# Optimization experiments

Measured on AMD Instinct MI355X. Metric: run time of the kernel, lower is better.

Reference implementation:

```python
import jax, jax.numpy as jnp
import numpy as np

MAX_FREQ = 4
OMEGA = 0.5 * np.pi
PATCH = 64


def _unnorm(c, size):
    # align_corners=False convention of torch.grid_sample
    return ((c + 1.0) * size - 1.0) / 2.0


def _gather(im, yy, xx):
    # im [C,H,W], yy/xx [Ho,Wo] -> [C,Ho,Wo]
    return im[:, yy, xx]


def _gs_nearest(inp, grid):
    # inp [B,C,H,W], grid [B,Ho,Wo,2] (x,y); padding_mode='border'
    B, C, H, W = inp.shape
    x = jnp.clip(jnp.round(_unnorm(grid[..., 0], W)), 0, W - 1).astype(jnp.int32)
    y = jnp.clip(jnp.round(_unnorm(grid[..., 1], H)), 0, H - 1).astype(jnp.int32)
    return jax.vmap(_gather)(inp, y, x)  # [B,C,Ho,Wo]


def _gs_bilinear(inp, grid):
    B, C, H, W = inp.shape
    x = jnp.clip(_unnorm(grid[..., 0], W), 0.0, W - 1.0)
    y = jnp.clip(_unnorm(grid[..., 1], H), 0.0, H - 1.0)
    x0 = jnp.floor(x); y0 = jnp.floor(y)
    wx = (x - x0)[:, None]; wy = (y - y0)[:, None]  # [B,1,Ho,Wo]
    x0i = x0.astype(jnp.int32); y0i = y0.astype(jnp.int32)
    x1i = jnp.minimum(x0i + 1, W - 1); y1i = jnp.minimum(y0i + 1, H - 1)
    g = jax.vmap(_gather)
    v00 = g(inp, y0i, x0i); v01 = g(inp, y0i, x1i)
    v10 = g(inp, y1i, x0i); v11 = g(inp, y1i, x1i)
    return (v00 * (1 - wx) * (1 - wy) + v01 * wx * (1 - wy)
            + v10 * (1 - wx) * wy + v11 * wx * wy)


def _conv2d(x, w, b):
    y = jax.lax.conv_general_dilated(x, w, (1, 1), ((1, 1), (1, 1)),
                                     dimension_numbers=("NCHW", "OIHW", "NCHW"))
    return y + b[None, :, None, None]


def _lc_decoder(q, rel):
    # q [B,Ho,Wo,2F+1], rel [B,Ho,Wo,1]; Fourier basis [1, cos(k*w*rel), sin(k*w*rel)]
    k = jnp.arange(1, MAX_FREQ + 1, dtype=q.dtype)
    ang = rel * k * OMEGA  # [B,Ho,Wo,F]
    basis = jnp.concatenate([jnp.ones_like(rel), jnp.cos(ang), jnp.sin(ang)], axis=-1)
    return jnp.sum(q * basis, axis=-1, keepdims=True)  # [B,Ho,Wo,1]


def _forward(sinogram, feat, grid, square_inv, adapt_w, adapt_b):
    B = feat.shape[0]
    sino = _conv2d(feat, adapt_w, adapt_b)          # [B,2F+1,V,D]
    V, D = sino.shape[-2], sino.shape[-1]
    # make_coord along detector axis (dim=1 coord channel), padding=0
    coord_d = ((jnp.arange(D, dtype=sino.dtype) + 0.5) / D) * 2.0 - 1.0
    sino_coord = jnp.broadcast_to(coord_d[None, None, None, :], (B, 1, V, D))
    shift_interval = 1.0 / D
    eps = 1e-4
    q_recons, lengths = [], []
    for sx in (-shift_interval, shift_interval):  # ensembling shifts
        g = grid + jnp.array([sx, 0.0], dtype=grid.dtype) + 1e-6
        q_recon = jnp.transpose(_gs_nearest(sino, g), (0, 2, 3, 1))       # [B,V,P2,2F+1]
        q_coord = jnp.transpose(_gs_nearest(sino_coord, g), (0, 2, 3, 1))  # [B,V,P2,1]
        rel = (grid[..., 0:1] - q_coord) * D
        q_recons.append(_lc_decoder(q_recon, rel))
        lengths.append(jnp.abs(rel) + eps)
    tot = lengths[0] + lengths[1]
    # lengths are swapped before weighting (cross weighting)
    recon = q_recons[0] * lengths[1] / tot + q_recons[1] * lengths[0] / tot
    out = jnp.sum(jnp.transpose(recon, (0, 3, 1, 2)) * square_inv * 10000.0, axis=-2)
    # back projection of center channel of raw sinogram
    ch = sinogram.shape[1]
    bp = _gs_bilinear(sinogram[:, ch // 2:ch // 2 + 1], grid)
    out = out + jnp.sum(bp * square_inv * 10000.0, axis=-2)  # [B,1,P2]
    return out.reshape(B, 1, PATCH, PATCH)


def setup_inputs() -> dict:
    key = jax.random.key(0)
    ks = jax.random.split(key, 6)
    B, V, D, ENC = 4, 360, 512, 64
    P2 = PATCH * PATCH
    CH = 2 * MAX_FREQ + 1
    return {
        "sinogram": jax.random.normal(ks[0], (B, 1, V, D), jnp.float32),
        "feat": jax.random.normal(ks[1], (B, ENC, V, D), jnp.float32),
        "grid": jax.random.uniform(ks[2], (B, V, P2, 2), jnp.float32, -1.0, 1.0),
        "square_inv": jax.random.uniform(ks[3], (B, 1, V, P2), jnp.float32, 1e-5, 1e-4),
        "adapt_w": jax.random.normal(ks[4], (CH, ENC, 3, 3), jnp.float32) * 0.05,
        "adapt_b": jax.random.normal(ks[5], (CH,), jnp.float32) * 0.05,
    }


def reference(sinogram, feat, grid, square_inv, adapt_w, adapt_b):
    return _forward(sinogram, feat, grid, square_inv, adapt_w, adapt_b)
```

## Files before the change

### kernel.cpp

```cpp
#include <hip/hip_runtime.h>
#include <hip/hip_fp16.h>
#include <math.h>

#define B   4
#define V   360
#define D   512
#define ENC 64
#define CH  9
#define P2  4096
#define NCHUNK 45
#define VCHUNK 8
#define DPT 8
#define RECH 16

__global__ __launch_bounds__(256) void conv_kernel(
    const float* __restrict__ feat,
    const float* __restrict__ w,
    const float* __restrict__ bias,
    __half* __restrict__ sino)
{
    const int bid = blockIdx.x;
    const int sw  = (bid & 7) * 45 + (bid >> 3);
    const int b   = sw / 90;
    const int vt  = sw % 90;
    const int tr  = threadIdx.x >> 6;
    const int v   = vt * 4 + tr;
    const int d0  = (threadIdx.x & 63) * DPT;

    float acc[CH][DPT];
    #pragma unroll
    for (int oc = 0; oc < CH; ++oc) {
        const float bv = bias[oc];
        #pragma unroll
        for (int p = 0; p < DPT; ++p) acc[oc][p] = bv;
    }

    const float* fb = feat + ((size_t)b * ENC * V + v) * D + d0;
    const bool vm = v > 0, vp = v < V - 1;
    const bool dm = d0 > 0, dp = (d0 + DPT) < D;

    for (int ic = 0; ic < ENC; ++ic) {
        const float* f = fb + (size_t)ic * (V * D);
        float r[3][DPT + 2];
        #pragma unroll
        for (int rr = 0; rr < 3; ++rr) {
            const float* fr = f + (rr - 1) * D;
            const bool ok = (rr == 0) ? vm : ((rr == 2) ? vp : true);
            float4 c0 = ok ? *(const float4*)fr       : float4{0.f, 0.f, 0.f, 0.f};
            float4 c1 = ok ? *(const float4*)(fr + 4) : float4{0.f, 0.f, 0.f, 0.f};
            r[rr][1] = c0.x; r[rr][2] = c0.y; r[rr][3] = c0.z; r[rr][4] = c0.w;
            r[rr][5] = c1.x; r[rr][6] = c1.y; r[rr][7] = c1.z; r[rr][8] = c1.w;
            r[rr][0]       = (ok && dm) ? fr[-1]   : 0.f;
            r[rr][DPT + 1] = (ok && dp) ? fr[DPT]  : 0.f;
        }
        #pragma unroll
        for (int oc = 0; oc < CH; ++oc) {
            const float* ww = w + ((size_t)oc * ENC + ic) * 9;
            #pragma unroll
            for (int kr = 0; kr < 3; ++kr) {
                #pragma unroll
                for (int kc = 0; kc < 3; ++kc) {
                    const float wv = ww[kr * 3 + kc];
                    #pragma unroll
                    for (int p = 0; p < DPT; ++p)
                        acc[oc][p] = fmaf(r[kr][p + kc], wv, acc[oc][p]);
                }
            }
        }
    }

    #pragma unroll
    for (int p = 0; p < DPT; ++p) {
        __half* rec = sino + (size_t)(((size_t)b * V + v) * D + d0 + p) * RECH;
        union { __half2 h; unsigned u; } cv;
        uint4 pk;
        cv.h = __floats2half2_rn(acc[0][p], acc[1][p]); pk.x = cv.u;
        cv.h = __floats2half2_rn(acc[2][p], acc[3][p]); pk.y = cv.u;
        cv.h = __floats2half2_rn(acc[4][p], acc[5][p]); pk.z = cv.u;
        cv.h = __floats2half2_rn(acc[6][p], acc[7][p]); pk.w = cv.u;
        *(uint4*)rec = pk;
        cv.h = __floats2half2_rn(acc[8][p], 0.f);
        *(unsigned*)(rec + 8) = cv.u;
    }
}

__device__ __forceinline__ void unpack9(const __half* rec, float* q)
{
    const uint4 a = *(const uint4*)rec;
    union { unsigned u; __half2 h; } c;
    float2 f;
    c.u = a.x; f = __half22float2(c.h); q[0] = f.x; q[1] = f.y;
    c.u = a.y; f = __half22float2(c.h); q[2] = f.x; q[3] = f.y;
    c.u = a.z; f = __half22float2(c.h); q[4] = f.x; q[5] = f.y;
    c.u = a.w; f = __half22float2(c.h); q[6] = f.x; q[7] = f.y;
    const unsigned e = *(const unsigned*)(rec + 8);
    union { unsigned short us; __half hh; } c2;
    c2.us = (unsigned short)e;
    q[8] = __half2float(c2.hh);
}

__device__ __forceinline__ float point_contrib(
    int b, int v, int p,
    const __half* __restrict__ sb, const float* __restrict__ sg,
    const float* __restrict__ grid, const float* __restrict__ sq)
{
    const size_t gi = (size_t)(b * V + v) * P2 + p;
    const double gd = __builtin_nontemporal_load((const double*)grid + gi);
    const unsigned long long gu = __double_as_longlong(gd);
    const float gx = __uint_as_float((unsigned)gu);
    const float gy = __uint_as_float((unsigned)(gu >> 32));
    const float s  = __builtin_nontemporal_load(sq + gi);

    const float fy = ((gy + 1e-6f + 1.f) * (float)V - 1.f) * 0.5f;
    const int   yi = (int)fminf(fmaxf(rintf(fy), 0.f), (float)(V - 1));
    const float fx0 = ((gx + 1e-6f + 1.f) * (float)D - 1.f) * 0.5f;

    float val[2], len[2];
    #pragma unroll
    for (int sft = 0; sft < 2; ++sft) {
        const float fx = (sft == 0) ? (fx0 - 0.5f) : (fx0 + 0.5f);
        const int   xi = (int)fminf(fmaxf(rintf(fx), 0.f), (float)(D - 1));
        const float qc = ((float)xi + 0.5f) * (2.f / (float)D) - 1.f;
        const float rel = (gx - qc) * (float)D;

        float q[9];
        unpack9(sb + (size_t)(yi * D + xi) * RECH, q);

        const float ang = rel * 1.5707963267948966f;
        float s1, c1;
        __sincosf(ang, &s1, &c1);
        const float c2 = fmaf(2.f * c1, c1, -1.f);
        const float s2 = 2.f * c1 * s1;
        const float c3 = fmaf(2.f * c1, c2, -c1);
        const float s3 = fmaf(2.f * c1, s2, -s1);
        const float c4 = fmaf(2.f * c1, c3, -c2);
        const float s4 = fmaf(2.f * c1, s3, -s2);

        float vv = q[0];
        vv = fmaf(q[1], c1, vv); vv = fmaf(q[2], c2, vv);
        vv = fmaf(q[3], c3, vv); vv = fmaf(q[4], c4, vv);
        vv = fmaf(q[5], s1, vv); vv = fmaf(q[6], s2, vv);
        vv = fmaf(q[7], s3, vv); vv = fmaf(q[8], s4, vv);
        val[sft] = vv;
        len[sft] = fabsf(rel) + 1e-4f;
    }
    const float tot   = len[0] + len[1];
    const float recon = (val[0] * len[1] + val[1] * len[0]) / tot;

    float fxb = fminf(fmaxf(((gx + 1.f) * (float)D - 1.f) * 0.5f, 0.f), (float)(D - 1));
    float fyb = fminf(fmaxf(((gy + 1.f) * (float)V - 1.f) * 0.5f, 0.f), (float)(V - 1));
    const float x0 = floorf(fxb), y0 = floorf(fyb);
    const float wx = fxb - x0,    wy = fyb - y0;
    const int x0i = (int)x0, y0i = (int)y0;
    const int x1i = min(x0i + 1, D - 1), y1i = min(y0i + 1, V - 1);
    const float v00 = sg[y0i * D + x0i], v01 = sg[y0i * D + x1i];
    const float v10 = sg[y1i * D + x0i], v11 = sg[y1i * D + x1i];
    const float bp = v00 * (1.f - wx) * (1.f - wy) + v01 * wx * (1.f - wy)
                   + v10 * (1.f - wx) * wy        + v11 * wx * wy;

    return (recon + bp) * s * 1e4f;
}

__global__ __launch_bounds__(256) void sample_kernel(
    const __half* __restrict__ sino,
    const float* __restrict__ sinogram,
    const float* __restrict__ grid,
    const float* __restrict__ sq,
    float* __restrict__ partial)
{
    const int bid = blockIdx.x;
    const int xcd = bid & 7;
    const int b   = xcd >> 1;
    const int idx = ((bid >> 3) << 1) | (xcd & 1);
    const int chunk = idx >> 4;
    const int p  = (idx & 15) * 256 + threadIdx.x;
    const int v0 = chunk * VCHUNK;

    const float* sg = sinogram + (size_t)b * V * D;
    const __half* sb = sino + (size_t)b * V * D * RECH;

    float acc = 0.f;
    #pragma unroll 1
    for (int v = v0; v < v0 + VCHUNK; v += 2) {
        const float c0 = point_contrib(b, v,     p, sb, sg, grid, sq);
        const float c1 = point_contrib(b, v + 1, p, sb, sg, grid, sq);
        acc += c0;
        acc += c1;
    }
    __builtin_nontemporal_store(acc, partial + ((size_t)chunk * B + b) * P2 + p);
}

__global__ __launch_bounds__(256) void reduce_kernel(
    const float* __restrict__ partial, float* __restrict__ out)
{
    const int i = blockIdx.x * 256 + threadIdx.x;
    float a = 0.f;
    #pragma unroll
    for (int c = 0; c < NCHUNK; ++c)
        a += __builtin_nontemporal_load(partial + (size_t)c * B * P2 + i);
    out[i] = a;
}

extern "C" void kernel_launch(void* const* d_in, const int* in_sizes, int n_in,
                              void* d_out, int out_size, void* d_ws, size_t ws_size,
                              hipStream_t stream)
{
    const float* sinogram = (const float*)d_in[0];
    const float* feat     = (const float*)d_in[1];
    const float* grid     = (const float*)d_in[2];
    const float* sq       = (const float*)d_in[3];
    const float* w        = (const float*)d_in[4];
    const float* bias     = (const float*)d_in[5];
    float* out = (float*)d_out;

    __half* sino    = (__half*)d_ws;
    float*  partial = (float*)((char*)d_ws + (size_t)B * V * D * RECH * sizeof(__half));

    conv_kernel<<<dim3(360), 256, 0, stream>>>(feat, w, bias, sino);
    sample_kernel<<<dim3(2880), 256, 0, stream>>>(sino, sinogram, grid, sq, partial);
    reduce_kernel<<<dim3((B * P2) / 256), 256, 0, stream>>>(partial, out);
}
```

Measured before the change: 297.4 us.

## Halve conv tile, batch sample loads, add paired bilinear sinogram table

The conv kernel now computes 4 detector positions per thread over 720 blocks instead of 8 over 360, giving more parallelism and fewer registers per thread. The sample kernel now handles 4 views per block and issues all grid, record and bilinear loads up front before any math, to expose memory-level parallelism. When the workspace is large enough, a precomputed float2 table pairs each sinogram texel with its right neighbour, so bilinear sampling needs two 8-byte loads instead of four scalar ones. This adds an extra kernel launch and doubles the number of partial sums the reduce kernel must read.

```diff
diff --git a/kernel.cpp b/kernel.cpp
--- a/kernel.cpp
+++ b/kernel.cpp
@@ -8,9 +8,9 @@
 #define ENC 64
 #define CH  9
 #define P2  4096
-#define NCHUNK 45
-#define VCHUNK 8
-#define DPT 8
+#define NCHUNK 90
+#define VCHUNK 4
+#define DPT 4
 #define RECH 16
 
 __global__ __launch_bounds__(256) void conv_kernel(
@@ -20,12 +20,12 @@
     __half* __restrict__ sino)
 {
     const int bid = blockIdx.x;
-    const int sw  = (bid & 7) * 45 + (bid >> 3);
-    const int b   = sw / 90;
-    const int vt  = sw % 90;
-    const int tr  = threadIdx.x >> 6;
-    const int v   = vt * 4 + tr;
-    const int d0  = (threadIdx.x & 63) * DPT;
+    const int sw  = (bid & 7) * 90 + (bid >> 3);
+    const int b   = sw / 180;
+    const int vt  = sw % 180;
+    const int tr  = threadIdx.x >> 7;
+    const int v   = vt * 2 + tr;
+    const int d0  = (threadIdx.x & 127) * DPT;
 
     float acc[CH][DPT];
     #pragma unroll
@@ -46,12 +46,10 @@
         for (int rr = 0; rr < 3; ++rr) {
             const float* fr = f + (rr - 1) * D;
             const bool ok = (rr == 0) ? vm : ((rr == 2) ? vp : true);
-            float4 c0 = ok ? *(const float4*)fr       : float4{0.f, 0.f, 0.f, 0.f};
-            float4 c1 = ok ? *(const float4*)(fr + 4) : float4{0.f, 0.f, 0.f, 0.f};
-            r[rr][1] = c0.x; r[rr][2] = c0.y; r[rr][3] = c0.z; r[rr][4] = c0.w;
-            r[rr][5] = c1.x; r[rr][6] = c1.y; r[rr][7] = c1.z; r[rr][8] = c1.w;
-            r[rr][0]       = (ok && dm) ? fr[-1]   : 0.f;
-            r[rr][DPT + 1] = (ok && dp) ? fr[DPT]  : 0.f;
+            float4 c = ok ? *(const float4*)fr : float4{0.f, 0.f, 0.f, 0.f};
+            r[rr][1] = c.x; r[rr][2] = c.y; r[rr][3] = c.z; r[rr][4] = c.w;
+            r[rr][0] = (ok && dm) ? fr[-1]  : 0.f;
+            r[rr][5] = (ok && dp) ? fr[DPT] : 0.f;
         }
         #pragma unroll
         for (int oc = 0; oc < CH; ++oc) {
@@ -84,86 +82,21 @@
     }
 }
 
-__device__ __forceinline__ void unpack9(const __half* rec, float* q)
-{
-    const uint4 a = *(const uint4*)rec;
-    union { unsigned u; __half2 h; } c;
-    float2 f;
-    c.u = a.x; f = __half22float2(c.h); q[0] = f.x; q[1] = f.y;
-    c.u = a.y; f = __half22float2(c.h); q[2] = f.x; q[3] = f.y;
-    c.u = a.z; f = __half22float2(c.h); q[4] = f.x; q[5] = f.y;
-    c.u = a.w; f = __half22float2(c.h); q[6] = f.x; q[7] = f.y;
-    const unsigned e = *(const unsigned*)(rec + 8);
-    union { unsigned short us; __half hh; } c2;
-    c2.us = (unsigned short)e;
-    q[8] = __half2float(c2.hh);
-}
-
-__device__ __forceinline__ float point_contrib(
-    int b, int v, int p,
-    const __half* __restrict__ sb, const float* __restrict__ sg,
-    const float* __restrict__ grid, const float* __restrict__ sq)
-{
-    const size_t gi = (size_t)(b * V + v) * P2 + p;
-    const double gd = __builtin_nontemporal_load((const double*)grid + gi);
-    const unsigned long long gu = __double_as_longlong(gd);
-    const float gx = __uint_as_float((unsigned)gu);
-    const float gy = __uint_as_float((unsigned)(gu >> 32));
-    const float s  = __builtin_nontemporal_load(sq + gi);
-
-    const float fy = ((gy + 1e-6f + 1.f) * (float)V - 1.f) * 0.5f;
-    const int   yi = (int)fminf(fmaxf(rintf(fy), 0.f), (float)(V - 1));
-    const float fx0 = ((gx + 1e-6f + 1.f) * (float)D - 1.f) * 0.5f;
-
-    float val[2], len[2];
-    #pragma unroll
-    for (int sft = 0; sft < 2; ++sft) {
-        const float fx = (sft == 0) ? (fx0 - 0.5f) : (fx0 + 0.5f);
-        const int   xi = (int)fminf(fmaxf(rintf(fx), 0.f), (float)(D - 1));
-        const float qc = ((float)xi + 0.5f) * (2.f / (float)D) - 1.f;
-        const float rel = (gx - qc) * (float)D;
-
-        float q[9];
-        unpack9(sb + (size_t)(yi * D + xi) * RECH, q);
-
-        const float ang = rel * 1.5707963267948966f;
-        float s1, c1;
-        __sincosf(ang, &s1, &c1);
-        const float c2 = fmaf(2.f * c1, c1, -1.f);
-        const float s2 = 2.f * c1 * s1;
-        const float c3 = fmaf(2.f * c1, c2, -c1);
-        const float s3 = fmaf(2.f * c1, s2, -s1);
-        const float c4 = fmaf(2.f * c1, c3, -c2);
-        const float s4 = fmaf(2.f * c1, s3, -s2);
-
-        float vv = q[0];
-        vv = fmaf(q[1], c1, vv); vv = fmaf(q[2], c2, vv);
-        vv = fmaf(q[3], c3, vv); vv = fmaf(q[4], c4, vv);
-        vv = fmaf(q[5], s1, vv); vv = fmaf(q[6], s2, vv);
-        vv = fmaf(q[7], s3, vv); vv = fmaf(q[8], s4, vv);
-        val[sft] = vv;
-        len[sft] = fabsf(rel) + 1e-4f;
-    }
-    const float tot   = len[0] + len[1];
-    const float recon = (val[0] * len[1] + val[1] * len[0]) / tot;
-
-    float fxb = fminf(fmaxf(((gx + 1.f) * (float)D - 1.f) * 0.5f, 0.f), (float)(D - 1));
-    float fyb = fminf(fmaxf(((gy + 1.f) * (float)V - 1.f) * 0.5f, 0.f), (float)(V - 1));
-    const float x0 = floorf(fxb), y0 = floorf(fyb);
-    const float wx = fxb - x0,    wy = fyb - y0;
-    const int x0i = (int)x0, y0i = (int)y0;
-    const int x1i = min(x0i + 1, D - 1), y1i = min(y0i + 1, V - 1);
-    const float v00 = sg[y0i * D + x0i], v01 = sg[y0i * D + x1i];
-    const float v10 = sg[y1i * D + x0i], v11 = sg[y1i * D + x1i];
-    const float bp = v00 * (1.f - wx) * (1.f - wy) + v01 * wx * (1.f - wy)
-                   + v10 * (1.f - wx) * wy        + v11 * wx * wy;
-
-    return (recon + bp) * s * 1e4f;
-}
-
+__global__ __launch_bounds__(256) void build_sg2(
+    const float* __restrict__ sg, float2* __restrict__ sg2)
+{
+    const int i = blockIdx.x * 256 + threadIdx.x;
+    const int x = i & (D - 1);
+    const float a = sg[i];
+    const float c = (x == D - 1) ? a : sg[i + 1];
+    sg2[i] = float2{a, c};
+}
+
+template <int PAIRED>
 __global__ __launch_bounds__(256) void sample_kernel(
     const __half* __restrict__ sino,
     const float* __restrict__ sinogram,
+    const float2* __restrict__ sg2,
     const float* __restrict__ grid,
     const float* __restrict__ sq,
     float* __restrict__ partial)
@@ -176,16 +109,108 @@
     const int p  = (idx & 15) * 256 + threadIdx.x;
     const int v0 = chunk * VCHUNK;
 
-    const float* sg = sinogram + (size_t)b * V * D;
-    const __half* sb = sino + (size_t)b * V * D * RECH;
+    const float*  sg  = sinogram + (size_t)b * V * D;
+    const float2* sg2b = sg2 + (size_t)b * V * D;
+    const __half* sb  = sino + (size_t)b * V * D * RECH;
+
+    float gx[4], gy[4], sv[4];
+    #pragma unroll
+    for (int u = 0; u < 4; ++u) {
+        const size_t gi = (size_t)(b * V + v0 + u) * P2 + p;
+        const double gd = __builtin_nontemporal_load((const double*)grid + gi);
+        const unsigned long long gu = __double_as_longlong(gd);
+        gx[u] = __uint_as_float((unsigned)gu);
+        gy[u] = __uint_as_float((unsigned)(gu >> 32));
+        sv[u] = __builtin_nontemporal_load(sq + gi);
+    }
+
+    uint4    ra[4][2];
+    unsigned rzu[4][2];
+    float    rel[4][2];
+    #pragma unroll
+    for (int u = 0; u < 4; ++u) {
+        const float fy = ((gy[u] + 1e-6f + 1.f) * (float)V - 1.f) * 0.5f;
+        const int   yi = (int)fminf(fmaxf(rintf(fy), 0.f), (float)(V - 1));
+        const float fx0 = ((gx[u] + 1e-6f + 1.f) * (float)D - 1.f) * 0.5f;
+        #pragma unroll
+        for (int sft = 0; sft < 2; ++sft) {
+            const float fx = (sft == 0) ? (fx0 - 0.5f) : (fx0 + 0.5f);
+            const int   xi = (int)fminf(fmaxf(rintf(fx), 0.f), (float)(D - 1));
+            const float qc = ((float)xi + 0.5f) * (2.f / (float)D) - 1.f;
+            rel[u][sft] = (gx[u] - qc) * (float)D;
+            const __half* rec = sb + (size_t)(yi * D + xi) * RECH;
+            ra[u][sft]  = *(const uint4*)rec;
+            rzu[u][sft] = *(const unsigned*)(rec + 8);
+        }
+    }
+
+    float bl00[4], bl01[4], bl10[4], bl11[4], wxv[4], wyv[4];
+    #pragma unroll
+    for (int u = 0; u < 4; ++u) {
+        float fxb = fminf(fmaxf(((gx[u] + 1.f) * (float)D - 1.f) * 0.5f, 0.f), (float)(D - 1));
+        float fyb = fminf(fmaxf(((gy[u] + 1.f) * (float)V - 1.f) * 0.5f, 0.f), (float)(V - 1));
+        const float x0 = floorf(fxb), y0 = floorf(fyb);
+        wxv[u] = fxb - x0; wyv[u] = fyb - y0;
+        const int x0i = (int)x0, y0i = (int)y0;
+        const int y1i = min(y0i + 1, V - 1);
+        if (PAIRED) {
+            const float2 t = sg2b[y0i * D + x0i];
+            const float2 u2 = sg2b[y1i * D + x0i];
+            bl00[u] = t.x;  bl01[u] = t.y;
+            bl10[u] = u2.x; bl11[u] = u2.y;
+        } else {
+            const int x1i = min(x0i + 1, D - 1);
+            bl00[u] = sg[y0i * D + x0i]; bl01[u] = sg[y0i * D + x1i];
+            bl10[u] = sg[y1i * D + x0i]; bl11[u] = sg[y1i * D + x1i];
+        }
+    }
 
     float acc = 0.f;
-    #pragma unroll 1
-    for (int v = v0; v < v0 + VCHUNK; v += 2) {
-        const float c0 = point_contrib(b, v,     p, sb, sg, grid, sq);
-        const float c1 = point_contrib(b, v + 1, p, sb, sg, grid, sq);
-        acc += c0;
-        acc += c1;
+    #pragma unroll
+    for (int u = 0; u < 4; ++u) {
+        float val[2], len[2];
+        #pragma unroll
+        for (int sft = 0; sft < 2; ++sft) {
+            float q[9];
+            {
+                const uint4 a = ra[u][sft];
+                union { unsigned uu; __half2 h; } c;
+                float2 f;
+                c.uu = a.x; f = __half22float2(c.h); q[0] = f.x; q[1] = f.y;
+                c.uu = a.y; f = __half22float2(c.h); q[2] = f.x; q[3] = f.y;
+                c.uu = a.z; f = __half22float2(c.h); q[4] = f.x; q[5] = f.y;
+                c.uu = a.w; f = __half22float2(c.h); q[6] = f.x; q[7] = f.y;
+                union { unsigned short us; __half hh; } c2;
+                c2.us = (unsigned short)rzu[u][sft];
+                q[8] = __half2float(c2.hh);
+            }
+            const float r = rel[u][sft];
+            const float ang = r * 1.5707963267948966f;
+            float s1, c1;
+            __sincosf(ang, &s1, &c1);
+            const float c2 = fmaf(2.f * c1, c1, -1.f);
+            const float s2 = 2.f * c1 * s1;
+            const float c3 = fmaf(2.f * c1, c2, -c1);
+            const float s3 = fmaf(2.f * c1, s2, -s1);
+            const float c4 = fmaf(2.f * c1, c3, -c2);
+            const float s4 = fmaf(2.f * c1, s3, -s2);
+
+            float vv = q[0];
+            vv = fmaf(q[1], c1, vv); vv = fmaf(q[2], c2, vv);
+            vv = fmaf(q[3], c3, vv); vv = fmaf(q[4], c4, vv);
+            vv = fmaf(q[5], s1, vv); vv = fmaf(q[6], s2, vv);
+            vv = fmaf(q[7], s3, vv); vv = fmaf(q[8], s4, vv);
+            val[sft] = vv;
+            len[sft] = fabsf(r) + 1e-4f;
+        }
+        const float tot   = len[0] + len[1];
+        const float recon = (val[0] * len[1] + val[1] * len[0]) / tot;
+
+        const float wx = wxv[u], wy = wyv[u];
+        const float bp = bl00[u] * (1.f - wx) * (1.f - wy) + bl01[u] * wx * (1.f - wy)
+                       + bl10[u] * (1.f - wx) * wy         + bl11[u] * wx * wy;
+
+        acc += (recon + bp) * sv[u] * 1e4f;
     }
     __builtin_nontemporal_store(acc, partial + ((size_t)chunk * B + b) * P2 + p);
 }
@@ -195,7 +220,7 @@
 {
     const int i = blockIdx.x * 256 + threadIdx.x;
     float a = 0.f;
-    #pragma unroll
+    #pragma unroll 6
     for (int c = 0; c < NCHUNK; ++c)
         a += __builtin_nontemporal_load(partial + (size_t)c * B * P2 + i);
     out[i] = a;
@@ -213,10 +238,21 @@
     const float* bias     = (const float*)d_in[5];
     float* out = (float*)d_out;
 
+    const size_t sino_b = (size_t)B * V * D * RECH * sizeof(__half);
+    const size_t part_b = (size_t)NCHUNK * B * P2 * sizeof(float);
+    const size_t sg2_b  = (size_t)B * V * D * sizeof(float2);
+
     __half* sino    = (__half*)d_ws;
-    float*  partial = (float*)((char*)d_ws + (size_t)B * V * D * RECH * sizeof(__half));
-
-    conv_kernel<<<dim3(360), 256, 0, stream>>>(feat, w, bias, sino);
-    sample_kernel<<<dim3(2880), 256, 0, stream>>>(sino, sinogram, grid, sq, partial);
+    float*  partial = (float*)((char*)d_ws + sino_b);
+    float2* sg2     = (float2*)((char*)d_ws + sino_b + part_b);
+    const bool paired = (ws_size >= sino_b + part_b + sg2_b);
+
+    conv_kernel<<<dim3(720), 256, 0, stream>>>(feat, w, bias, sino);
+    if (paired) {
+        build_sg2<<<dim3(2880), 256, 0, stream>>>(sinogram, sg2);
+        sample_kernel<1><<<dim3(5760), 256, 0, stream>>>(sino, sinogram, sg2, grid, sq, partial);
+    } else {
+        sample_kernel<0><<<dim3(5760), 256, 0, stream>>>(sino, sinogram, sg2, grid, sq, partial);
+    }
     reduce_kernel<<<dim3((B * P2) / 256), 256, 0, stream>>>(partial, out);
 }
```

After: 278.3 us. -6.4%, faster.
